# Kernel optimization log

Hardware: AMD Instinct MI355X
Metric: run time of the kernel (lower is better)

Reference implementation:

```python
import jax, jax.numpy as jnp
import numpy as np

BATCH, T, D_MODEL, DIM = 8, 4096, 512, 512
R_MIN, R_MAX, MAX_PHASE = 0.0, 1.0, 6.28


def setup_inputs() -> dict:
    key = jax.random.key(0)
    ks = jax.random.split(key, 8)
    x = jax.random.normal(ks[0], (BATCH, T, D_MODEL), dtype=jnp.float32)
    h0 = jnp.zeros((BATCH, 1, DIM), dtype=jnp.float32)
    # nu_log / theta_log per the module's initializers
    u1 = jax.random.uniform(ks[1], (DIM,))
    nu_log = jnp.log(-0.5 * jnp.log(u1 * (R_MAX ** 2 - R_MIN ** 2) + R_MIN ** 2)).astype(jnp.float32)
    u2 = jax.random.uniform(ks[2], (DIM,))
    theta_log = jnp.log(MAX_PHASE * u2).astype(jnp.float32)
    # B ~ N(0,1)/sqrt(2*D_in), C ~ N(0,1)/sqrt(D_out)
    B_re = (jax.random.normal(ks[3], (D_MODEL, DIM)) / jnp.sqrt(2.0 * D_MODEL)).astype(jnp.float32)
    B_im = (jax.random.normal(ks[4], (D_MODEL, DIM)) / jnp.sqrt(2.0 * D_MODEL)).astype(jnp.float32)
    C_re = (jax.random.normal(ks[5], (DIM, D_MODEL)) / jnp.sqrt(float(D_MODEL))).astype(jnp.float32)
    C_im = (jax.random.normal(ks[6], (DIM, D_MODEL)) / jnp.sqrt(float(D_MODEL))).astype(jnp.float32)
    D_param = jax.random.normal(ks[7], (D_MODEL,)).astype(jnp.float32)
    # gamma_log = log(sqrt(1 - |Lambda|^2)) with Lambda from nu/theta
    diag_lambda = jnp.exp(-jnp.exp(nu_log) + 1j * jnp.exp(theta_log))
    gamma_log = jnp.log(jnp.sqrt(1.0 - jnp.abs(diag_lambda) ** 2)).astype(jnp.float32)
    return {"x": x, "h0": h0, "nu_log": nu_log, "theta_log": theta_log,
            "B_re": B_re, "B_im": B_im, "C_re": C_re, "C_im": C_im,
            "D_param": D_param, "gamma_log": gamma_log}


def _binary_op(ei, ej):
    a_i, b_i = ei
    a_j, b_j = ej
    return (a_j * a_i, a_j * b_i + b_j)


def reference(x, h0, nu_log, theta_log, B_re, B_im, C_re, C_im, D_param, gamma_log):
    B, T_len, _ = x.shape
    Lambda = jnp.exp(-jnp.exp(nu_log) + 1j * jnp.exp(theta_log))            # (N,) complex
    B_norm = (B_re + 1j * B_im) * jnp.exp(gamma_log)[None, :]               # (D,N) complex
    C = C_re + 1j * C_im                                                     # (N,D) complex
    # Input projection: Bu[b,t,n] = sum_d x[b,t,d] * B_norm[d,n]
    Bu = jnp.einsum('btd,dn->btn', x.astype(jnp.complex64), B_norm)
    Bu = jnp.concatenate([h0.astype(jnp.complex64), Bu], axis=1)             # (B,T+1,N)
    Lam = jnp.broadcast_to(Lambda, Bu.shape)                                 # (B,T+1,N)
    _, H = jax.lax.associative_scan(_binary_op, (Lam, Bu), axis=1)
    H = H[:, 1:]                                                             # (B,T,N)
    y = jnp.einsum('btn,nd->btd', H, C).real + D_param * x                   # (B,T,D)
    new_h = H[:, -1:]                                                        # (B,1,N) complex
    return (y, new_h)
```

## Files before the change

### kernel.cpp

```cpp
#include <hip/hip_runtime.h>

#define T_LEN 4096
#define DMODEL 512
#define DIM 512
#define NBATCH 8
#define MROWS (NBATCH * T_LEN)
#define NCHUNK 128
#define LCHUNK 32

typedef __attribute__((ext_vector_type(8))) short short8;
typedef __attribute__((ext_vector_type(4))) float float4v;

__device__ __forceinline__ ushort f2b(float f) {
    union { float fl; unsigned u; } v; v.fl = f;
    unsigned u = v.u;
    return (ushort)((u + 0x7FFFu + ((u >> 16) & 1u)) >> 16);
}
__device__ __forceinline__ float b2f(ushort u) {
    union { unsigned u; float f; } v; v.u = (unsigned)u << 16; return v.f;
}

__device__ __forceinline__ void glds16(const ushort* g, ushort* l) {
    __builtin_amdgcn_global_load_lds(
        (const __attribute__((address_space(1))) void*)g,
        (__attribute__((address_space(3))) void*)l, 16, 0, 0);
}

#define XBLK (MROWS * 512 / 4 / 256)
#define TBLK 256

__global__ __launch_bounds__(256) void k_prep(const float* __restrict__ x,
                                              const float* __restrict__ B_re,
                                              const float* __restrict__ B_im,
                                              const float* __restrict__ gamma_log,
                                              const float* __restrict__ C_re,
                                              const float* __restrict__ C_im,
                                              ushort* __restrict__ Xb,
                                              ushort* __restrict__ BT,
                                              ushort* __restrict__ CT) {
    __shared__ float T[64][65];
    int bb = blockIdx.x;
    if (bb < XBLK) {
        int i = (bb * 256 + threadIdx.x) * 4;
        float4 v = *(const float4*)(x + i);
        ushort4 o;
        o.x = f2b(v.x); o.y = f2b(v.y); o.z = f2b(v.z); o.w = f2b(v.w);
        *(ushort4*)(Xb + i) = o;
        return;
    }
    int tb = bb - XBLK;
    int mat = tb >> 6;
    int tile = tb & 63;
    int r0 = (tile >> 3) * 64;
    int c0 = (tile & 7) * 64;
    const float* IN = (mat == 0) ? B_re : (mat == 1) ? B_im : (mat == 2) ? C_re : C_im;
    int lr_ = threadIdx.x & 63;
    int lc  = threadIdx.x >> 6;
#pragma unroll
    for (int p = 0; p < 16; p++)
        T[4 * p + lc][lr_] = IN[(size_t)(c0 + 4 * p + lc) * 512 + r0 + lr_];
    __syncthreads();
#pragma unroll
    for (int p = 0; p < 16; p++) {
        int rr = 4 * p + lc;
        int r = r0 + rr;
        float v = T[lr_][rr];
        if (mat <= 1) {
            v *= __expf(gamma_log[r]);
            BT[(size_t)(mat * 512 + r) * 512 + c0 + lr_] = f2b(v);
        } else {
            if (mat == 3) v = -v;
            CT[(size_t)r * 1024 + (mat - 2) * 512 + c0 + lr_] = f2b(v);
        }
    }
}

template<int K, int MODE, int NBN>
__global__ __launch_bounds__(256) void k_gemm(
    const ushort* __restrict__ A, const ushort* __restrict__ Bt,
    ushort* __restrict__ oRe, ushort* __restrict__ oIm,
    float* __restrict__ y, const float* __restrict__ x, const float* __restrict__ Dp) {
    __shared__ ushort sA[128 * 64];
    __shared__ ushort sB[128 * 64];
    const int tid = threadIdx.x;
    const int L = blockIdx.x;
    const int xcd = L & 7;
    const int slot = L >> 3;
    const int m0 = (xcd * 32 + slot / NBN) * 128;
    const int n0 = (slot % NBN) * 128;
    const int wave = tid >> 6;
    const int lane = tid & 63;
    const int wm = (wave >> 1) * 64;
    const int wn = (wave & 1) * 64;
    const int lr = lane & 15;
    const int quad = lane >> 4;

    const int srow = lane >> 3;
    const int schunk = (lane & 7) ^ srow;
    const ushort* gA0 = A + (size_t)(m0 + wave * 32 + srow) * K + schunk * 8;
    const ushort* gB0 = Bt + (size_t)(n0 + wave * 32 + srow) * K + schunk * 8;

    float4v acc[4][4];
#pragma unroll
    for (int i = 0; i < 4; i++)
#pragma unroll
        for (int j = 0; j < 4; j++) {
            float4v z = {0.f, 0.f, 0.f, 0.f};
            acc[i][j] = z;
        }

    for (int k0 = 0; k0 < K; k0 += 64) {
        __syncthreads();
#pragma unroll
        for (int c = 0; c < 4; c++) {
            glds16(gA0 + (size_t)(c * 8) * K + k0, &sA[(wave * 32 + c * 8) * 64]);
            glds16(gB0 + (size_t)(c * 8) * K + k0, &sB[(wave * 32 + c * 8) * 64]);
        }
        __syncthreads();

#pragma unroll
        for (int kk = 0; kk < 2; kk++) {
            short8 af[4], bfr[4];
#pragma unroll
            for (int i = 0; i < 4; i++) {
                int row = wm + i * 16 + lr;
                af[i] = *(const short8*)&sA[row * 64 + (((kk * 4 + quad) ^ (row & 7)) * 8)];
            }
#pragma unroll
            for (int j = 0; j < 4; j++) {
                int row = wn + j * 16 + lr;
                bfr[j] = *(const short8*)&sB[row * 64 + (((kk * 4 + quad) ^ (row & 7)) * 8)];
            }
#pragma unroll
            for (int i = 0; i < 4; i++)
#pragma unroll
                for (int j = 0; j < 4; j++)
                    acc[i][j] = __builtin_amdgcn_mfma_f32_16x16x32_bf16(af[i], bfr[j], acc[i][j], 0, 0, 0);
        }
    }

#pragma unroll
    for (int i = 0; i < 4; i++) {
#pragma unroll
        for (int j = 0; j < 4; j++) {
            int gmb = m0 + wm + i * 16 + quad * 4;
            int gn = n0 + wn + j * 16 + lr;
#pragma unroll
            for (int r = 0; r < 4; r++) {
                float v = acc[i][j][r];
                int row = gmb + r;
                if (MODE == 1) {
                    if (gn < 512) oRe[(size_t)row * 512 + gn] = f2b(v);
                    else oIm[(size_t)row * 512 + (gn - 512)] = f2b(v);
                } else {
                    size_t o = (size_t)row * 512 + gn;
                    y[o] = v + Dp[gn] * x[o];
                }
            }
        }
    }
}


__device__ __forceinline__ void lambda_of(const float* nu_log, const float* theta_log,
                                          int n, float& lre, float& lim) {
    float e = __expf(nu_log[n]);
    float th = __expf(theta_log[n]);
    float rad = __expf(-e);
    float s, c;
    __sincosf(th, &s, &c);
    lre = rad * c;
    lim = rad * s;
}

__global__ __launch_bounds__(256) void k_scan1(const ushort* __restrict__ BuRe,
                                               const ushort* __restrict__ BuIm,
                                               const float* __restrict__ nu_log,
                                               const float* __restrict__ theta_log,
                                               float* __restrict__ cRe, float* __restrict__ cIm) {
    int n2 = threadIdx.x;
    int b = blockIdx.x >> 7;
    int c = blockIdx.x & 127;
    float lre0, lim0, lre1, lim1;
    lambda_of(nu_log, theta_log, 2 * n2, lre0, lim0);
    lambda_of(nu_log, theta_log, 2 * n2 + 1, lre1, lim1);
    float hr0 = 0.f, hi0 = 0.f, hr1 = 0.f, hi1 = 0.f;
    size_t base = ((size_t)b * T_LEN + (size_t)c * LCHUNK) * 512 + 2 * n2;
#pragma unroll 8
    for (int j = 0; j < LCHUNK; j++) {
        ushort2 ur = *(const ushort2*)(BuRe + base + (size_t)j * 512);
        ushort2 ui = *(const ushort2*)(BuIm + base + (size_t)j * 512);
        float br0 = b2f(ur.x), br1 = b2f(ur.y), bi0 = b2f(ui.x), bi1 = b2f(ui.y);
        float nr0 = lre0 * hr0 - lim0 * hi0 + br0;
        float ni0 = lre0 * hi0 + lim0 * hr0 + bi0;
        hr0 = nr0; hi0 = ni0;
        float nr1 = lre1 * hr1 - lim1 * hi1 + br1;
        float ni1 = lre1 * hi1 + lim1 * hr1 + bi1;
        hr1 = nr1; hi1 = ni1;
    }
    size_t co = ((size_t)b * NCHUNK + c) * 512 + 2 * n2;
    *(float2*)(cRe + co) = make_float2(hr0, hr1);
    *(float2*)(cIm + co) = make_float2(hi0, hi1);
}

__global__ __launch_bounds__(256) void k_scanB(const ushort* __restrict__ BuRe,
                                               const ushort* __restrict__ BuIm,
                                               const float* __restrict__ cRe,
                                               const float* __restrict__ cIm,
                                               const float* __restrict__ h0,
                                               const float* __restrict__ nu_log,
                                               const float* __restrict__ theta_log,
                                               ushort* __restrict__ Hbf,
                                               float* __restrict__ newH, int newh_mode) {
    int n2 = threadIdx.x;
    int b = blockIdx.x >> 7;
    int c = blockIdx.x & 127;
    float lre0, lim0, lre1, lim1;
    lambda_of(nu_log, theta_log, 2 * n2, lre0, lim0);
    lambda_of(nu_log, theta_log, 2 * n2 + 1, lre1, lim1);
    float Lr0 = lre0, Li0 = lim0, Lr1 = lre1, Li1 = lim1;
#pragma unroll
    for (int s = 0; s < 5; s++) {
        float a0 = Lr0 * Lr0 - Li0 * Li0, q0 = 2.f * Lr0 * Li0; Lr0 = a0; Li0 = q0;
        float a1 = Lr1 * Lr1 - Li1 * Li1, q1 = 2.f * Lr1 * Li1; Lr1 = a1; Li1 = q1;
    }
    float fr0 = h0[b * 512 + 2 * n2], fi0 = 0.f;
    float fr1 = h0[b * 512 + 2 * n2 + 1], fi1 = 0.f;
    size_t cb = (size_t)b * NCHUNK * 512 + 2 * n2;
#pragma unroll 4
    for (int j = 0; j < c; j++) {
        float2 ar = *(const float2*)(cRe + cb + (size_t)j * 512);
        float2 ai = *(const float2*)(cIm + cb + (size_t)j * 512);
        float nr0 = Lr0 * fr0 - Li0 * fi0 + ar.x;
        float ni0 = Lr0 * fi0 + Li0 * fr0 + ai.x;
        fr0 = nr0; fi0 = ni0;
        float nr1 = Lr1 * fr1 - Li1 * fi1 + ar.y;
        float ni1 = Lr1 * fi1 + Li1 * fr1 + ai.y;
        fr1 = nr1; fi1 = ni1;
    }
    if (c == NCHUNK - 1) {
        float2 ar = *(const float2*)(cRe + cb + (size_t)(NCHUNK - 1) * 512);
        float2 ai = *(const float2*)(cIm + cb + (size_t)(NCHUNK - 1) * 512);
        float cr0 = Lr0 * fr0 - Li0 * fi0 + ar.x;
        float ci0 = Lr0 * fi0 + Li0 * fr0 + ai.x;
        float cr1 = Lr1 * fr1 - Li1 * fi1 + ar.y;
        float ci1 = Lr1 * fi1 + Li1 * fr1 + ai.y;
        size_t i0 = (size_t)b * 512 + 2 * n2;
        if (newh_mode == 1) {
            newH[i0] = cr0; newH[i0 + 1] = cr1;
            newH[(size_t)NBATCH * 512 + i0] = ci0;
            newH[(size_t)NBATCH * 512 + i0 + 1] = ci1;
        } else if (newh_mode == 2) {
            newH[i0] = cr0; newH[i0 + 1] = cr1;
        } else {
            newH[i0 * 2] = cr0; newH[i0 * 2 + 1] = ci0;
            newH[(i0 + 1) * 2] = cr1; newH[(i0 + 1) * 2 + 1] = ci1;
        }
    }
    float pr0 = lre0, pi0 = lim0, pr1 = lre1, pi1 = lim1;
    float hr0 = 0.f, hi0 = 0.f, hr1 = 0.f, hi1 = 0.f;
    size_t row0 = (size_t)b * T_LEN + (size_t)c * LCHUNK;
#pragma unroll 4
    for (int j = 0; j < LCHUNK; j++) {
        size_t base = (row0 + j) * 512 + 2 * n2;
        ushort2 ur = *(const ushort2*)(BuRe + base);
        ushort2 ui = *(const ushort2*)(BuIm + base);
        float br0 = b2f(ur.x), br1 = b2f(ur.y), bi0 = b2f(ui.x), bi1 = b2f(ui.y);
        float nr0 = lre0 * hr0 - lim0 * hi0 + br0;
        float ni0 = lre0 * hi0 + lim0 * hr0 + bi0;
        hr0 = nr0; hi0 = ni0;
        float nr1 = lre1 * hr1 - lim1 * hi1 + br1;
        float ni1 = lre1 * hi1 + lim1 * hr1 + bi1;
        hr1 = nr1; hi1 = ni1;
        float vr0 = hr0 + pr0 * fr0 - pi0 * fi0;
        float vi0 = hi0 + pr0 * fi0 + pi0 * fr0;
        float vr1 = hr1 + pr1 * fr1 - pi1 * fi1;
        float vi1 = hi1 + pr1 * fi1 + pi1 * fr1;
        size_t hrow = (row0 + j) * 1024;
        ushort2 wre, wim;
        wre.x = f2b(vr0); wre.y = f2b(vr1);
        wim.x = f2b(vi0); wim.y = f2b(vi1);
        *(ushort2*)(Hbf + hrow + 2 * n2) = wre;
        *(ushort2*)(Hbf + hrow + 512 + 2 * n2) = wim;
        float npr0 = pr0 * lre0 - pi0 * lim0;
        float npi0 = pr0 * lim0 + pi0 * lre0;
        pr0 = npr0; pi0 = npi0;
        float npr1 = pr1 * lre1 - pi1 * lim1;
        float npi1 = pr1 * lim1 + pi1 * lre1;
        pr1 = npr1; pi1 = npi1;
    }
}


extern "C" void kernel_launch(void* const* d_in, const int* in_sizes, int n_in,
                              void* d_out, int out_size, void* d_ws, size_t ws_size,
                              hipStream_t stream) {
    const float* x         = (const float*)d_in[0];
    const float* h0        = (const float*)d_in[1];
    const float* nu_log    = (const float*)d_in[2];
    const float* theta_log = (const float*)d_in[3];
    const float* B_re      = (const float*)d_in[4];
    const float* B_im      = (const float*)d_in[5];
    const float* C_re      = (const float*)d_in[6];
    const float* C_im      = (const float*)d_in[7];
    const float* D_param   = (const float*)d_in[8];
    const float* gamma_log = (const float*)d_in[9];

    char* ws = (char*)d_ws;
    size_t off = 0;
    ushort* Xb   = (ushort*)(ws + off); off += (size_t)MROWS * 512 * 2;
    ushort* BT   = (ushort*)(ws + off); off += (size_t)1024 * 512 * 2;
    ushort* CT   = (ushort*)(ws + off); off += (size_t)512 * 1024 * 2;
    ushort* BuRe = (ushort*)(ws + off); off += (size_t)MROWS * 512 * 2;
    ushort* BuIm = (ushort*)(ws + off); off += (size_t)MROWS * 512 * 2;
    ushort* Hbf  = (ushort*)(ws + off); off += (size_t)MROWS * 1024 * 2;
    float*  cRe  = (float*)(ws + off); off += (size_t)NBATCH * NCHUNK * 512 * 4;
    float*  cIm  = (float*)(ws + off); off += (size_t)NBATCH * NCHUNK * 512 * 4;

    float* y_out = (float*)d_out;
    float* newH  = (float*)d_out + (size_t)MROWS * 512;

    const int tail = out_size - MROWS * 512;
    int newh_mode = 0;
    if (tail == NBATCH * 512 * 2) newh_mode = 1;
    else if (tail == NBATCH * 512) newh_mode = 2;

    k_prep<<<dim3(XBLK + TBLK), dim3(256), 0, stream>>>(
        x, B_re, B_im, gamma_log, C_re, C_im, Xb, BT, CT);

    k_gemm<512, 1, 8><<<dim3(2048), dim3(256), 0, stream>>>(
        Xb, BT, BuRe, BuIm, nullptr, nullptr, nullptr);

    k_scan1<<<dim3(NBATCH * NCHUNK), dim3(256), 0, stream>>>(BuRe, BuIm, nu_log, theta_log, cRe, cIm);
    k_scanB<<<dim3(NBATCH * NCHUNK), dim3(256), 0, stream>>>(
        BuRe, BuIm, cRe, cIm, h0, nu_log, theta_log, Hbf, newH, newh_mode);

    k_gemm<1024, 2, 4><<<dim3(1024), dim3(256), 0, stream>>>(
        Hbf, CT, nullptr, nullptr, y_out, x, D_param);
}
```

Baseline: 285.7 us.

## Replace GEMM with 256x256-tile, 8-wave kernel using double-buffered async LDS prefetch

Both GEMMs now run through a new kernel with 512 threads and 256x256 output tiles, which halves or quarters the grid size. Global-to-LDS loads are double-buffered and split into K halves, and each is issued while MFMAs run on the previous buffer. The schedule is coordinated with explicit barriers, vmcnt waits and setprio. The aim is to hide memory latency and get more reuse per loaded tile. In exchange it uses more registers and LDS per block (64KB), and the small grids (512 and 256 blocks) may leave CUs underused or poorly balanced.

```diff
diff --git a/kernel.cpp b/kernel.cpp
--- a/kernel.cpp
+++ b/kernel.cpp
@@ -75,76 +75,102 @@
     }
 }
 
+
 template<int K, int MODE, int NBN>
-__global__ __launch_bounds__(256) void k_gemm(
+__global__ __launch_bounds__(512) void k_gemm8(
     const ushort* __restrict__ A, const ushort* __restrict__ Bt,
     ushort* __restrict__ oRe, ushort* __restrict__ oIm,
     float* __restrict__ y, const float* __restrict__ x, const float* __restrict__ Dp) {
-    __shared__ ushort sA[128 * 64];
-    __shared__ ushort sB[128 * 64];
+    const int NT = K / 64;
+    __shared__ ushort sA[2][2][8192];
+    __shared__ ushort sB[2][2][8192];
     const int tid = threadIdx.x;
     const int L = blockIdx.x;
     const int xcd = L & 7;
     const int slot = L >> 3;
-    const int m0 = (xcd * 32 + slot / NBN) * 128;
-    const int n0 = (slot % NBN) * 128;
+    const int m0 = (xcd * 16 + slot / NBN) * 256;
+    const int n0 = (slot % NBN) * 256;
     const int wave = tid >> 6;
     const int lane = tid & 63;
-    const int wm = (wave >> 1) * 64;
-    const int wn = (wave & 1) * 64;
+    const int wmid = wave >> 2;
+    const int wnid = wave & 3;
     const int lr = lane & 15;
     const int quad = lane >> 4;
 
-    const int srow = lane >> 3;
-    const int schunk = (lane & 7) ^ srow;
-    const ushort* gA0 = A + (size_t)(m0 + wave * 32 + srow) * K + schunk * 8;
-    const ushort* gB0 = Bt + (size_t)(n0 + wave * 32 + srow) * K + schunk * 8;
-
-    float4v acc[4][4];
-#pragma unroll
-    for (int i = 0; i < 4; i++)
+    const int sr = wave * 16 + (lane >> 2);
+    const int sc = (lane & 3) ^ (sr & 3);
+    const ushort* gAs = A  + (size_t)(m0 + sr) * K + sc * 8;
+    const ushort* gBs = Bt + (size_t)(n0 + sr) * K + sc * 8;
+
+    const int xorq = (quad ^ (lr & 3)) * 8;
+    const int aBase = (wmid * 128 + lr) * 32 + xorq;
+    const int bBase = (wnid * 64 + lr) * 32 + xorq;
+
+    float4v acc[8][4];
+#pragma unroll
+    for (int i = 0; i < 8; i++)
 #pragma unroll
         for (int j = 0; j < 4; j++) {
             float4v z = {0.f, 0.f, 0.f, 0.f};
             acc[i][j] = z;
         }
 
-    for (int k0 = 0; k0 < K; k0 += 64) {
-        __syncthreads();
-#pragma unroll
-        for (int c = 0; c < 4; c++) {
-            glds16(gA0 + (size_t)(c * 8) * K + k0, &sA[(wave * 32 + c * 8) * 64]);
-            glds16(gB0 + (size_t)(c * 8) * K + k0, &sB[(wave * 32 + c * 8) * 64]);
-        }
-        __syncthreads();
-
-#pragma unroll
-        for (int kk = 0; kk < 2; kk++) {
-            short8 af[4], bfr[4];
-#pragma unroll
-            for (int i = 0; i < 4; i++) {
-                int row = wm + i * 16 + lr;
-                af[i] = *(const short8*)&sA[row * 64 + (((kk * 4 + quad) ^ (row & 7)) * 8)];
-            }
-#pragma unroll
-            for (int j = 0; j < 4; j++) {
-                int row = wn + j * 16 + lr;
-                bfr[j] = *(const short8*)&sB[row * 64 + (((kk * 4 + quad) ^ (row & 7)) * 8)];
-            }
-#pragma unroll
-            for (int i = 0; i < 4; i++)
-#pragma unroll
-                for (int j = 0; j < 4; j++)
-                    acc[i][j] = __builtin_amdgcn_mfma_f32_16x16x32_bf16(af[i], bfr[j], acc[i][j], 0, 0, 0);
-        }
-    }
-
-#pragma unroll
-    for (int i = 0; i < 4; i++) {
+#define STG(gM, sM, kt, kh, buf) do { \
+        glds16((gM) + (kt) * 64 + (kh) * 32, &sM[buf][kh][wave * 512]); \
+        glds16((gM) + (size_t)128 * K + (kt) * 64 + (kh) * 32, &sM[buf][kh][wave * 512 + 4096]); \
+    } while (0)
+
+#define PH(AH, BH, MH, DOSTG, STGEXPR, VMEXPR) do { \
+        short8 af_[4], bf_[4]; \
+        _Pragma("unroll") for (int i_ = 0; i_ < 4; i_++) \
+            af_[i_] = *(const short8*)&(AH)[aBase + ((MH) * 4 + i_) * 512]; \
+        _Pragma("unroll") for (int j_ = 0; j_ < 4; j_++) \
+            bf_[j_] = *(const short8*)&(BH)[bBase + j_ * 512]; \
+        if (DOSTG) { STGEXPR; } \
+        __builtin_amdgcn_s_barrier(); \
+        asm volatile("s_waitcnt lgkmcnt(0)" ::: "memory"); \
+        __builtin_amdgcn_sched_barrier(0); \
+        __builtin_amdgcn_s_setprio(1); \
+        _Pragma("unroll") for (int i_ = 0; i_ < 4; i_++) \
+        _Pragma("unroll") for (int j_ = 0; j_ < 4; j_++) \
+            acc[(MH) * 4 + i_][j_] = __builtin_amdgcn_mfma_f32_16x16x32_bf16( \
+                af_[i_], bf_[j_], acc[(MH) * 4 + i_][j_], 0, 0, 0); \
+        __builtin_amdgcn_s_setprio(0); \
+        VMEXPR; \
+        __builtin_amdgcn_s_barrier(); \
+    } while (0)
+
+    STG(gAs, sA, 0, 0, 0); STG(gBs, sB, 0, 0, 0);
+    STG(gAs, sA, 0, 1, 0); STG(gBs, sB, 0, 1, 0);
+    STG(gAs, sA, 1, 0, 1); STG(gBs, sB, 1, 0, 1);
+    asm volatile("s_waitcnt vmcnt(4)" ::: "memory");
+    __builtin_amdgcn_s_barrier();
+
+    for (int t = 0; t < NT; t += 2) {
+        const bool s2 = (t + 2 < NT);
+        const bool s3 = (t + 3 < NT);
+        PH(sA[0][0], sB[0][0], 0, true, STG(gAs, sA, t + 1, 1, 1), (void)0);
+        PH(sA[0][0], sB[0][0], 1, true, STG(gBs, sB, t + 1, 1, 1), (void)0);
+        PH(sA[0][1], sB[0][1], 0, s2, STG(gAs, sA, t + 2, 0, 0), (void)0);
+        PH(sA[0][1], sB[0][1], 1, s2, STG(gBs, sB, t + 2, 0, 0),
+           if (s2) { asm volatile("s_waitcnt vmcnt(4)" ::: "memory"); }
+           else    { asm volatile("s_waitcnt vmcnt(0)" ::: "memory"); });
+        PH(sA[1][0], sB[1][0], 0, s2, STG(gAs, sA, t + 2, 1, 0), (void)0);
+        PH(sA[1][0], sB[1][0], 1, s2, STG(gBs, sB, t + 2, 1, 0), (void)0);
+        PH(sA[1][1], sB[1][1], 0, s3, STG(gAs, sA, t + 3, 0, 1), (void)0);
+        PH(sA[1][1], sB[1][1], 1, s3, STG(gBs, sB, t + 3, 0, 1),
+           if (s3) { asm volatile("s_waitcnt vmcnt(4)" ::: "memory"); }
+           else    { asm volatile("s_waitcnt vmcnt(0)" ::: "memory"); });
+    }
+#undef PH
+#undef STG
+
+#pragma unroll
+    for (int i = 0; i < 8; i++) {
 #pragma unroll
         for (int j = 0; j < 4; j++) {
-            int gmb = m0 + wm + i * 16 + quad * 4;
-            int gn = n0 + wn + j * 16 + lr;
+            int gmb = m0 + wmid * 128 + i * 16 + quad * 4;
+            int gn = n0 + wnid * 64 + j * 16 + lr;
 #pragma unroll
             for (int r = 0; r < 4; r++) {
                 float v = acc[i][j][r];
@@ -328,13 +354,13 @@
     k_prep<<<dim3(XBLK + TBLK), dim3(256), 0, stream>>>(
         x, B_re, B_im, gamma_log, C_re, C_im, Xb, BT, CT);
 
-    k_gemm<512, 1, 8><<<dim3(2048), dim3(256), 0, stream>>>(
+    k_gemm8<512, 1, 4><<<dim3(512), dim3(512), 0, stream>>>(
         Xb, BT, BuRe, BuIm, nullptr, nullptr, nullptr);
 
     k_scan1<<<dim3(NBATCH * NCHUNK), dim3(256), 0, stream>>>(BuRe, BuIm, nu_log, theta_log, cRe, cIm);
     k_scanB<<<dim3(NBATCH * NCHUNK), dim3(256), 0, stream>>>(
         BuRe, BuIm, cRe, cIm, h0, nu_log, theta_log, Hbf, newH, newh_mode);
 
-    k_gemm<1024, 2, 4><<<dim3(1024), dim3(256), 0, stream>>>(
+    k_gemm8<1024, 2, 2><<<dim3(256), dim3(512), 0, stream>>>(
         Hbf, CT, nullptr, nullptr, y_out, x, D_param);
 }
```

Result: slower. 294.9 us (+3.2%).
